# Kernel optimization log

Hardware: AMD Instinct MI355X
Metric: run time of the kernel (lower is better)

## Reference

```python
import jax, jax.numpy as jnp
import numpy as np

B, T, D = 64, 256, 1024   # batch, seq_len, input_dim (== hidden_dim)
H = 1024                  # hidden_dim
L = 4                     # layer_dim
O = 512                   # output_dim


def setup_inputs() -> dict:
    key = jax.random.key(0)
    ks = jax.random.split(key, 8)
    s = 1.0 / np.sqrt(H)  # torch LSTMCell default init scale
    u = lambda k, shape: jax.random.uniform(k, shape, jnp.float32, -s, s)
    return {
        "x": jax.random.normal(ks[0], (B, T, D), jnp.float32),
        "W_ih": u(ks[1], (L, 4 * H, D)),   # layer 0 input dim == H
        "W_hh": u(ks[2], (L, 4 * H, H)),
        "b_ih": u(ks[3], (L, 4 * H)),
        "b_hh": u(ks[4], (L, 4 * H)),
        "W_fc": u(ks[5], (O, H)),
        "b_fc": u(ks[6], (O,)),
    }


def _lstm_forward(x, W_ih, W_hh, b_ih, b_hh, W_fc, b_fc):
    def step(carry, x_t):
        h, c = carry  # each [L, B, H]
        inp = x_t     # [B, D]
        for l in range(L):
            gates = inp @ W_ih[l].T + b_ih[l] + h[l] @ W_hh[l].T + b_hh[l]  # [B, 4H]
            i, f, g, o = jnp.split(gates, 4, axis=-1)
            i, f, o = jax.nn.sigmoid(i), jax.nn.sigmoid(f), jax.nn.sigmoid(o)
            g = jnp.tanh(g)
            c_new = f * c[l] + i * g
            h_new = o * jnp.tanh(c_new)
            h = h.at[l].set(h_new)
            c = c.at[l].set(c_new)
            inp = h_new
        return (h, c), None

    h0 = jnp.zeros((L, x.shape[0], H), x.dtype)
    c0 = jnp.zeros((L, x.shape[0], H), x.dtype)
    (h, _), _ = jax.lax.scan(step, (h0, c0), jnp.swapaxes(x, 0, 1))  # scan over time
    return h[-1] @ W_fc.T + b_fc  # [B, O]


def reference(x, W_ih, W_hh, b_ih, b_hh, W_fc, b_fc):
    return _lstm_forward(x, W_ih, W_hh, b_ih, b_hh, W_fc, b_fc)
```

## Files before the change

kernel.cpp:

```cpp
#include <hip/hip_runtime.h>


typedef short           bf16x8 __attribute__((ext_vector_type(8)));
typedef unsigned short  u16x8  __attribute__((ext_vector_type(8)));
typedef float           f32x4  __attribute__((ext_vector_type(4)));

static constexpr int kB  = 64;
static constexpr int kT  = 256;
static constexpr int kH  = 1024;
static constexpr int kL  = 4;
static constexpr int kNG = 4096;
static constexpr int kK2 = 2048;

static constexpr size_t OFF_W    = 0;
static constexpr size_t OFF_BIAS = 67108864;
static constexpr size_t OFF_XB   = 67174400;
static constexpr size_t OFF_H    = 100728832;
static constexpr size_t OFF_C    = 101777408;

static __device__ __forceinline__ unsigned short f2bf(float f) {
  unsigned int u = __float_as_uint(f);
  u += 0x7fffu + ((u >> 16) & 1u);
  return (unsigned short)(u >> 16);
}
static __device__ __forceinline__ float bf2f(unsigned short s) {
  return __uint_as_float(((unsigned int)s) << 16);
}
static __device__ __forceinline__ float sigm_(float x) {
  return 1.0f / (1.0f + __expf(-x));
}
static __device__ __forceinline__ float tanh_(float x) {
  return 1.0f - 2.0f / (__expf(2.0f * x) + 1.0f);
}

__global__ __launch_bounds__(256) void prepack_w(const float* __restrict__ Wih,
                                                 const float* __restrict__ Whh,
                                                 unsigned short* __restrict__ Wcat) {
  const size_t total = (size_t)kL * kNG * kK2;
  for (size_t e = (size_t)blockIdx.x * 256 + threadIdx.x; e < total;
       e += (size_t)gridDim.x * 256) {
    int k = (int)(e & 2047);
    int n = (int)((e >> 11) & 4095);
    int l = (int)(e >> 23);
    int r = (n & 3) * 1024 + (n >> 2);
    float v = (k < 1024) ? Wih[((size_t)l * kNG + r) * 1024 + k]
                         : Whh[((size_t)l * kNG + r) * 1024 + (k - 1024)];
    Wcat[e] = f2bf(v);
  }
}

__global__ __launch_bounds__(256) void prepack_bias(const float* __restrict__ bih,
                                                    const float* __restrict__ bhh,
                                                    float* __restrict__ bias) {
  int e = blockIdx.x * 256 + threadIdx.x;
  int l = e >> 12, n = e & 4095;
  int r = (n & 3) * 1024 + (n >> 2);
  bias[e] = bih[l * kNG + r] + bhh[l * kNG + r];
}

__global__ __launch_bounds__(256) void prepack_x(const float* __restrict__ x,
                                                 unsigned short* __restrict__ xb) {
  size_t e = ((size_t)blockIdx.x * 256 + threadIdx.x) * 8;
  float4 f0 = *(const float4*)(x + e);
  float4 f1 = *(const float4*)(x + e + 4);
  u16x8 v;
  v[0] = f2bf(f0.x); v[1] = f2bf(f0.y); v[2] = f2bf(f0.z); v[3] = f2bf(f0.w);
  v[4] = f2bf(f1.x); v[5] = f2bf(f1.y); v[6] = f2bf(f1.z); v[7] = f2bf(f1.w);
  *(u16x8*)(xb + e) = v;
}

__global__ __launch_bounds__(256) void lstm_diag(
    const unsigned short* __restrict__ Wcat, const float* __restrict__ bias,
    const unsigned short* __restrict__ xb, unsigned short* __restrict__ hbuf,
    float* __restrict__ cbuf, int d) {
  const int l = blockIdx.x >> 6;
  const int t = d - l;
  if (t < 0 || t >= kT) return;
  const int nwg = (blockIdx.x & 63) * 64;

  const int tid  = threadIdx.x;
  const int lane = tid & 63;
  const int w    = tid >> 6;
  const int quad = lane >> 4;
  const int l15  = lane & 15;

  const unsigned short* srcA;
  size_t strideA;
  if (w < 2) {
    if (l == 0) { srcA = xb + (size_t)t * kH + w * 512; strideA = (size_t)kT * kH; }
    else {
      srcA = hbuf + (size_t)((t & 1) * kL + (l - 1)) * (kB * kH) + w * 512;
      strideA = kH;
    }
  } else {
    srcA = hbuf + (size_t)(((t + 1) & 1) * kL + l) * (kB * kH) + (w - 2) * 512;
    strideA = kH;
  }

  const unsigned short* pA[4];
  const unsigned short* pB[4];
  {
    const unsigned short* wrow =
        Wcat + ((size_t)(l * kNG + nwg + l15)) * kK2 + w * 512 + quad * 8;
#pragma unroll
    for (int i = 0; i < 4; ++i) {
      pA[i] = srcA + (size_t)(i * 16 + l15) * strideA + quad * 8;
      pB[i] = wrow + (size_t)i * 16 * kK2;
    }
  }

  f32x4 acc[4][4] = {};
  bf16x8 a0[4], b0[4], a1[4], b1[4];

#pragma unroll
  for (int i = 0; i < 4; ++i) { a0[i] = *(const bf16x8*)(pA[i]); b0[i] = *(const bf16x8*)(pB[i]); }

#pragma unroll
  for (int kc = 0; kc < 16; ++kc) {
    bf16x8* ac = (kc & 1) ? a1 : a0;
    bf16x8* bc = (kc & 1) ? b1 : b0;
    bf16x8* an = (kc & 1) ? a0 : a1;
    bf16x8* bn = (kc & 1) ? b0 : b1;
    if (kc < 15) {
#pragma unroll
      for (int i = 0; i < 4; ++i) {
        an[i] = *(const bf16x8*)(pA[i] + (kc + 1) * 32);
        bn[i] = *(const bf16x8*)(pB[i] + (kc + 1) * 32);
      }
    }
#pragma unroll
    for (int mt = 0; mt < 4; ++mt)
#pragma unroll
      for (int nt = 0; nt < 4; ++nt)
        acc[mt][nt] = __builtin_amdgcn_mfma_f32_16x16x32_bf16(ac[mt], bc[nt],
                                                              acc[mt][nt], 0, 0, 0);
  }

  __shared__ float part[2][64][68];

  if (w >= 2) {
    float* p = &part[w - 2][0][0];
#pragma unroll
    for (int mt = 0; mt < 4; ++mt)
#pragma unroll
      for (int nt = 0; nt < 4; ++nt)
#pragma unroll
        for (int r = 0; r < 4; ++r)
          p[(mt * 16 + quad * 4 + r) * 68 + nt * 16 + l15] = acc[mt][nt][r];
  }
  __syncthreads();
  if (w < 2) {
    const float* p = &part[w][0][0];
#pragma unroll
    for (int mt = 0; mt < 4; ++mt)
#pragma unroll
      for (int nt = 0; nt < 4; ++nt)
#pragma unroll
        for (int r = 0; r < 4; ++r)
          acc[mt][nt][r] += p[(mt * 16 + quad * 4 + r) * 68 + nt * 16 + l15];
  }
  __syncthreads();
  if (w < 2) {
    float* p = &part[w][0][0];
#pragma unroll
    for (int mt = 0; mt < 4; ++mt)
#pragma unroll
      for (int nt = 0; nt < 4; ++nt)
#pragma unroll
        for (int r = 0; r < 4; ++r)
          p[(mt * 16 + quad * 4 + r) * 68 + nt * 16 + l15] = acc[mt][nt][r];
  }
  __syncthreads();

  const int m  = (w << 4) | (lane >> 2);
  const int ug = lane & 3;
  unsigned short* hout = hbuf + (size_t)((t & 1) * kL + l) * (kB * kH);
#pragma unroll
  for (int j = 0; j < 4; ++j) {
    int ul = 4 * j + ug;
    int nb = 4 * ul;
    float4 p0 = *(const float4*)&part[0][m][nb];
    float4 p1 = *(const float4*)&part[1][m][nb];
    float4 bs = *(const float4*)&bias[l * kNG + nwg + nb];
    float gi = sigm_(p0.x + p1.x + bs.x);
    float gf = sigm_(p0.y + p1.y + bs.y);
    float gg = tanh_(p0.z + p1.z + bs.z);
    float go = sigm_(p0.w + p1.w + bs.w);
    int u = (nwg >> 2) + ul;
    size_t ci = ((size_t)l * kB + m) * kH + u;
    float cn = gf * cbuf[ci] + gi * gg;
    cbuf[ci] = cn;
    hout[(size_t)m * kH + u] = f2bf(go * tanh_(cn));
  }
}

__global__ __launch_bounds__(256) void lstm_fc(const unsigned short* __restrict__ h3,
                                               const float* __restrict__ Wfc,
                                               const float* __restrict__ bfc,
                                               float* __restrict__ out) {
  int gt = blockIdx.x * 256 + threadIdx.x;
  int b = gt >> 9, o = gt & 511;
  const unsigned short* hr = h3 + (size_t)b * kH;
  const float* wr = Wfc + (size_t)o * kH;
  float acc = bfc[o];
#pragma unroll 4
  for (int k = 0; k < kH; k += 8) {
    u16x8 hv = *(const u16x8*)(hr + k);
    float4 w0 = *(const float4*)(wr + k);
    float4 w1 = *(const float4*)(wr + k + 4);
    acc += bf2f(hv[0]) * w0.x + bf2f(hv[1]) * w0.y + bf2f(hv[2]) * w0.z +
           bf2f(hv[3]) * w0.w + bf2f(hv[4]) * w1.x + bf2f(hv[5]) * w1.y +
           bf2f(hv[6]) * w1.z + bf2f(hv[7]) * w1.w;
  }
  out[gt] = acc;
}

extern "C" void kernel_launch(void* const* d_in, const int* in_sizes, int n_in,
                              void* d_out, int out_size, void* d_ws, size_t ws_size,
                              hipStream_t stream) {
  (void)in_sizes; (void)n_in; (void)out_size; (void)ws_size;
  const float* x   = (const float*)d_in[0];
  const float* Wih = (const float*)d_in[1];
  const float* Whh = (const float*)d_in[2];
  const float* bih = (const float*)d_in[3];
  const float* bhh = (const float*)d_in[4];
  const float* Wfc = (const float*)d_in[5];
  const float* bfc = (const float*)d_in[6];
  float* out = (float*)d_out;

  char* ws = (char*)d_ws;
  unsigned short* Wcat = (unsigned short*)(ws + OFF_W);
  float*          bias = (float*)(ws + OFF_BIAS);
  unsigned short* xb   = (unsigned short*)(ws + OFF_XB);
  unsigned short* hbuf = (unsigned short*)(ws + OFF_H);
  float*          cbuf = (float*)(ws + OFF_C);

  prepack_w<<<8192, 256, 0, stream>>>(Wih, Whh, Wcat);
  prepack_bias<<<64, 256, 0, stream>>>(bih, bhh, bias);
  prepack_x<<<8192, 256, 0, stream>>>(x, xb);
  hipMemsetAsync(ws + OFF_H, 0, 2097152, stream);

  for (int d = 0; d < kT + kL - 1; ++d)
    lstm_diag<<<256, 256, 0, stream>>>(Wcat, bias, xb, hbuf, cbuf, d);

  lstm_fc<<<128, 256, 0, stream>>>(hbuf + (size_t)7 * kB * kH, Wfc, bfc, out);
}
```

Before: 5.969 ms.

## Replace per-diagonal launches with persistent register-resident-weight LSTM kernel using flag sync

```diff
diff --git a/kernel.cpp b/kernel.cpp
--- a/kernel.cpp
+++ b/kernel.cpp
@@ -10,52 +10,21 @@
 static constexpr int kH  = 1024;
 static constexpr int kL  = 4;
 static constexpr int kNG = 4096;
-static constexpr int kK2 = 2048;
-
-static constexpr size_t OFF_W    = 0;
-static constexpr size_t OFF_BIAS = 67108864;
-static constexpr size_t OFF_XB   = 67174400;
-static constexpr size_t OFF_H    = 100728832;
-static constexpr size_t OFF_C    = 101777408;
+
+static constexpr size_t OFF_XB   = 0;
+static constexpr size_t OFF_H    = 33554432;
+static constexpr size_t OFF_FLAG = 35651584;
 
 static __device__ __forceinline__ unsigned short f2bf(float f) {
   unsigned int u = __float_as_uint(f);
   u += 0x7fffu + ((u >> 16) & 1u);
   return (unsigned short)(u >> 16);
 }
-static __device__ __forceinline__ float bf2f(unsigned short s) {
-  return __uint_as_float(((unsigned int)s) << 16);
-}
 static __device__ __forceinline__ float sigm_(float x) {
   return 1.0f / (1.0f + __expf(-x));
 }
 static __device__ __forceinline__ float tanh_(float x) {
   return 1.0f - 2.0f / (__expf(2.0f * x) + 1.0f);
-}
-
-__global__ __launch_bounds__(256) void prepack_w(const float* __restrict__ Wih,
-                                                 const float* __restrict__ Whh,
-                                                 unsigned short* __restrict__ Wcat) {
-  const size_t total = (size_t)kL * kNG * kK2;
-  for (size_t e = (size_t)blockIdx.x * 256 + threadIdx.x; e < total;
-       e += (size_t)gridDim.x * 256) {
-    int k = (int)(e & 2047);
-    int n = (int)((e >> 11) & 4095);
-    int l = (int)(e >> 23);
-    int r = (n & 3) * 1024 + (n >> 2);
-    float v = (k < 1024) ? Wih[((size_t)l * kNG + r) * 1024 + k]
-                         : Whh[((size_t)l * kNG + r) * 1024 + (k - 1024)];
-    Wcat[e] = f2bf(v);
-  }
-}
-
-__global__ __launch_bounds__(256) void prepack_bias(const float* __restrict__ bih,
-                                                    const float* __restrict__ bhh,
-                                                    float* __restrict__ bias) {
-  int e = blockIdx.x * 256 + threadIdx.x;
-  int l = e >> 12, n = e & 4095;
-  int r = (n & 3) * 1024 + (n >> 2);
-  bias[e] = bih[l * kNG + r] + bhh[l * kNG + r];
 }
 
 __global__ __launch_bounds__(256) void prepack_x(const float* __restrict__ x,
@@ -69,128 +38,174 @@
   *(u16x8*)(xb + e) = v;
 }
 
-__global__ __launch_bounds__(256) void lstm_diag(
-    const unsigned short* __restrict__ Wcat, const float* __restrict__ bias,
+__global__ __launch_bounds__(256, 1) void lstm_persist(
+    const float* __restrict__ Wih, const float* __restrict__ Whh,
+    const float* __restrict__ bih, const float* __restrict__ bhh,
     const unsigned short* __restrict__ xb, unsigned short* __restrict__ hbuf,
-    float* __restrict__ cbuf, int d) {
-  const int l = blockIdx.x >> 6;
-  const int t = d - l;
-  if (t < 0 || t >= kT) return;
-  const int nwg = (blockIdx.x & 63) * 64;
-
+    int* __restrict__ flags) {
+  const int l    = blockIdx.x >> 6;
+  const int nwg  = (blockIdx.x & 63) * 64;
   const int tid  = threadIdx.x;
   const int lane = tid & 63;
   const int w    = tid >> 6;
   const int quad = lane >> 4;
   const int l15  = lane & 15;
 
-  const unsigned short* srcA;
-  size_t strideA;
-  if (w < 2) {
-    if (l == 0) { srcA = xb + (size_t)t * kH + w * 512; strideA = (size_t)kT * kH; }
-    else {
-      srcA = hbuf + (size_t)((t & 1) * kL + (l - 1)) * (kB * kH) + w * 512;
-      strideA = kH;
-    }
-  } else {
-    srcA = hbuf + (size_t)(((t + 1) & 1) * kL + l) * (kB * kH) + (w - 2) * 512;
-    strideA = kH;
-  }
-
-  const unsigned short* pA[4];
-  const unsigned short* pB[4];
+  __shared__ float part[2][64][68];
+  __shared__ float cst[16][66];
+
+  for (int i = tid; i < 16 * 66; i += 256) (&cst[0][0])[i] = 0.0f;
+
+  bf16x8 wreg[16][4];
   {
-    const unsigned short* wrow =
-        Wcat + ((size_t)(l * kNG + nwg + l15)) * kK2 + w * 512 + quad * 8;
-#pragma unroll
-    for (int i = 0; i < 4; ++i) {
-      pA[i] = srcA + (size_t)(i * 16 + l15) * strideA + quad * 8;
-      pB[i] = wrow + (size_t)i * 16 * kK2;
-    }
-  }
-
-  f32x4 acc[4][4] = {};
-  bf16x8 a0[4], b0[4], a1[4], b1[4];
-
-#pragma unroll
-  for (int i = 0; i < 4; ++i) { a0[i] = *(const bf16x8*)(pA[i]); b0[i] = *(const bf16x8*)(pB[i]); }
-
-#pragma unroll
-  for (int kc = 0; kc < 16; ++kc) {
-    bf16x8* ac = (kc & 1) ? a1 : a0;
-    bf16x8* bc = (kc & 1) ? b1 : b0;
-    bf16x8* an = (kc & 1) ? a0 : a1;
-    bf16x8* bn = (kc & 1) ? b0 : b1;
-    if (kc < 15) {
-#pragma unroll
-      for (int i = 0; i < 4; ++i) {
-        an[i] = *(const bf16x8*)(pA[i] + (kc + 1) * 32);
-        bn[i] = *(const bf16x8*)(pB[i] + (kc + 1) * 32);
+    const float* Wsrc = (w < 2) ? Wih : Whh;
+    const int kofs = (w < 2) ? w * 512 : (w - 2) * 512;
+#pragma unroll
+    for (int nt = 0; nt < 4; ++nt) {
+      int n = nwg + nt * 16 + l15;
+      int r = (n & 3) * 1024 + (n >> 2);
+      const float* src = Wsrc + ((size_t)l * kNG + r) * 1024 + kofs + quad * 8;
+#pragma unroll
+      for (int kc = 0; kc < 16; ++kc) {
+        float4 f0 = *(const float4*)(src + kc * 32);
+        float4 f1 = *(const float4*)(src + kc * 32 + 4);
+        bf16x8 v;
+        v[0] = (short)f2bf(f0.x); v[1] = (short)f2bf(f0.y);
+        v[2] = (short)f2bf(f0.z); v[3] = (short)f2bf(f0.w);
+        v[4] = (short)f2bf(f1.x); v[5] = (short)f2bf(f1.y);
+        v[6] = (short)f2bf(f1.z); v[7] = (short)f2bf(f1.w);
+        wreg[kc][nt] = v;
       }
     }
-#pragma unroll
-    for (int mt = 0; mt < 4; ++mt)
-#pragma unroll
-      for (int nt = 0; nt < 4; ++nt)
-        acc[mt][nt] = __builtin_amdgcn_mfma_f32_16x16x32_bf16(ac[mt], bc[nt],
-                                                              acc[mt][nt], 0, 0, 0);
-  }
-
-  __shared__ float part[2][64][68];
-
-  if (w >= 2) {
-    float* p = &part[w - 2][0][0];
-#pragma unroll
-    for (int mt = 0; mt < 4; ++mt)
-#pragma unroll
-      for (int nt = 0; nt < 4; ++nt)
-#pragma unroll
-        for (int r = 0; r < 4; ++r)
-          p[(mt * 16 + quad * 4 + r) * 68 + nt * 16 + l15] = acc[mt][nt][r];
-  }
-  __syncthreads();
-  if (w < 2) {
-    const float* p = &part[w][0][0];
-#pragma unroll
-    for (int mt = 0; mt < 4; ++mt)
-#pragma unroll
-      for (int nt = 0; nt < 4; ++nt)
-#pragma unroll
-        for (int r = 0; r < 4; ++r)
-          acc[mt][nt][r] += p[(mt * 16 + quad * 4 + r) * 68 + nt * 16 + l15];
-  }
-  __syncthreads();
-  if (w < 2) {
-    float* p = &part[w][0][0];
-#pragma unroll
-    for (int mt = 0; mt < 4; ++mt)
-#pragma unroll
-      for (int nt = 0; nt < 4; ++nt)
-#pragma unroll
-        for (int r = 0; r < 4; ++r)
-          p[(mt * 16 + quad * 4 + r) * 68 + nt * 16 + l15] = acc[mt][nt][r];
-  }
-  __syncthreads();
-
-  const int m  = (w << 4) | (lane >> 2);
-  const int ug = lane & 3;
-  unsigned short* hout = hbuf + (size_t)((t & 1) * kL + l) * (kB * kH);
+  }
+
+  const int m_ep = (w << 4) | (lane >> 2);
+  const int ug   = lane & 3;
+  float4 bs4[4];
 #pragma unroll
   for (int j = 0; j < 4; ++j) {
-    int ul = 4 * j + ug;
-    int nb = 4 * ul;
-    float4 p0 = *(const float4*)&part[0][m][nb];
-    float4 p1 = *(const float4*)&part[1][m][nb];
-    float4 bs = *(const float4*)&bias[l * kNG + nwg + nb];
-    float gi = sigm_(p0.x + p1.x + bs.x);
-    float gf = sigm_(p0.y + p1.y + bs.y);
-    float gg = tanh_(p0.z + p1.z + bs.z);
-    float go = sigm_(p0.w + p1.w + bs.w);
-    int u = (nwg >> 2) + ul;
-    size_t ci = ((size_t)l * kB + m) * kH + u;
-    float cn = gf * cbuf[ci] + gi * gg;
-    cbuf[ci] = cn;
-    hout[(size_t)m * kH + u] = f2bf(go * tanh_(cn));
+    int u = (nwg >> 2) + 4 * j + ug;
+    bs4[j].x = bih[l * kNG + u]        + bhh[l * kNG + u];
+    bs4[j].y = bih[l * kNG + 1024 + u] + bhh[l * kNG + 1024 + u];
+    bs4[j].z = bih[l * kNG + 2048 + u] + bhh[l * kNG + 2048 + u];
+    bs4[j].w = bih[l * kNG + 3072 + u] + bhh[l * kNG + 3072 + u];
+  }
+
+  for (int t = 0; t < kT; ++t) {
+    if (l > 0) {
+      const int idx = (l - 1) * kT + t;
+      while (__hip_atomic_load(&flags[idx], __ATOMIC_RELAXED,
+                               __HIP_MEMORY_SCOPE_AGENT) < 64)
+        __builtin_amdgcn_s_sleep(1);
+      (void)__hip_atomic_load(&flags[idx], __ATOMIC_ACQUIRE,
+                              __HIP_MEMORY_SCOPE_AGENT);
+    }
+    if (t > 0) {
+      const int idx = l * kT + t - 1;
+      while (__hip_atomic_load(&flags[idx], __ATOMIC_RELAXED,
+                               __HIP_MEMORY_SCOPE_AGENT) < 64)
+        __builtin_amdgcn_s_sleep(1);
+      (void)__hip_atomic_load(&flags[idx], __ATOMIC_ACQUIRE,
+                              __HIP_MEMORY_SCOPE_AGENT);
+    }
+    if (l < 3 && t >= 4) {
+      const int idx = (l + 1) * kT + t - 4;
+      while (__hip_atomic_load(&flags[idx], __ATOMIC_RELAXED,
+                               __HIP_MEMORY_SCOPE_AGENT) < 64)
+        __builtin_amdgcn_s_sleep(1);
+      (void)__hip_atomic_load(&flags[idx], __ATOMIC_ACQUIRE,
+                              __HIP_MEMORY_SCOPE_AGENT);
+    }
+
+    f32x4 acc[4][4] = {};
+    const bool active = (w < 2) || (t > 0);
+    if (active) {
+      const unsigned short* srcA;
+      size_t strideA;
+      if (w < 2) {
+        if (l == 0) {
+          srcA = xb + (size_t)t * kH + w * 512;
+          strideA = (size_t)kT * kH;
+        } else {
+          srcA = hbuf + (size_t)((t & 3) * kL + (l - 1)) * (kB * kH) + w * 512;
+          strideA = kH;
+        }
+      } else {
+        srcA = hbuf + (size_t)(((t - 1) & 3) * kL + l) * (kB * kH) + (w - 2) * 512;
+        strideA = kH;
+      }
+      const unsigned short* pA[4];
+#pragma unroll
+      for (int i = 0; i < 4; ++i)
+        pA[i] = srcA + (size_t)(i * 16 + l15) * strideA + quad * 8;
+
+      bf16x8 abuf[4][4];
+#pragma unroll
+      for (int p = 0; p < 3; ++p)
+#pragma unroll
+        for (int i = 0; i < 4; ++i)
+          abuf[p][i] = *(const bf16x8*)(pA[i] + p * 32);
+#pragma unroll
+      for (int kc = 0; kc < 16; ++kc) {
+        if (kc < 13) {
+#pragma unroll
+          for (int i = 0; i < 4; ++i)
+            abuf[(kc + 3) & 3][i] = *(const bf16x8*)(pA[i] + (kc + 3) * 32);
+        }
+#pragma unroll
+        for (int mt = 0; mt < 4; ++mt)
+#pragma unroll
+          for (int nt = 0; nt < 4; ++nt)
+            acc[mt][nt] = __builtin_amdgcn_mfma_f32_16x16x32_bf16(
+                abuf[kc & 3][mt], wreg[kc][nt], acc[mt][nt], 0, 0, 0);
+      }
+    }
+
+    if (w >= 2) {
+      float* p = &part[w - 2][0][0];
+#pragma unroll
+      for (int mt = 0; mt < 4; ++mt)
+#pragma unroll
+        for (int nt = 0; nt < 4; ++nt)
+#pragma unroll
+          for (int r = 0; r < 4; ++r)
+            p[(mt * 16 + quad * 4 + r) * 68 + nt * 16 + l15] = acc[mt][nt][r];
+    }
+    __syncthreads();
+    if (w < 2) {
+      float* p = &part[w][0][0];
+#pragma unroll
+      for (int mt = 0; mt < 4; ++mt)
+#pragma unroll
+        for (int nt = 0; nt < 4; ++nt)
+#pragma unroll
+          for (int r = 0; r < 4; ++r) {
+            int a = (mt * 16 + quad * 4 + r) * 68 + nt * 16 + l15;
+            p[a] += acc[mt][nt][r];
+          }
+    }
+    __syncthreads();
+
+    unsigned short* hout = hbuf + (size_t)((t & 3) * kL + l) * (kB * kH);
+#pragma unroll
+    for (int j = 0; j < 4; ++j) {
+      int ul = 4 * j + ug;
+      int nb = 4 * ul;
+      float4 p0 = *(const float4*)&part[0][m_ep][nb];
+      float4 p1 = *(const float4*)&part[1][m_ep][nb];
+      float gi = sigm_(p0.x + p1.x + bs4[j].x);
+      float gf = sigm_(p0.y + p1.y + bs4[j].y);
+      float gg = tanh_(p0.z + p1.z + bs4[j].z);
+      float go = sigm_(p0.w + p1.w + bs4[j].w);
+      float cn = gf * cst[ul][m_ep] + gi * gg;
+      cst[ul][m_ep] = cn;
+      hout[(size_t)m_ep * kH + (nwg >> 2) + ul] = f2bf(go * tanh_(cn));
+    }
+
+    __syncthreads();
+    if (tid == 0)
+      __hip_atomic_fetch_add(&flags[l * kT + t], 1, __ATOMIC_RELEASE,
+                             __HIP_MEMORY_SCOPE_AGENT);
   }
 }
 
@@ -208,9 +223,14 @@
     u16x8 hv = *(const u16x8*)(hr + k);
     float4 w0 = *(const float4*)(wr + k);
     float4 w1 = *(const float4*)(wr + k + 4);
-    acc += bf2f(hv[0]) * w0.x + bf2f(hv[1]) * w0.y + bf2f(hv[2]) * w0.z +
-           bf2f(hv[3]) * w0.w + bf2f(hv[4]) * w1.x + bf2f(hv[5]) * w1.y +
-           bf2f(hv[6]) * w1.z + bf2f(hv[7]) * w1.w;
+    acc += __uint_as_float((unsigned)hv[0] << 16) * w0.x +
+           __uint_as_float((unsigned)hv[1] << 16) * w0.y +
+           __uint_as_float((unsigned)hv[2] << 16) * w0.z +
+           __uint_as_float((unsigned)hv[3] << 16) * w0.w +
+           __uint_as_float((unsigned)hv[4] << 16) * w1.x +
+           __uint_as_float((unsigned)hv[5] << 16) * w1.y +
+           __uint_as_float((unsigned)hv[6] << 16) * w1.z +
+           __uint_as_float((unsigned)hv[7] << 16) * w1.w;
   }
   out[gt] = acc;
 }
@@ -229,19 +249,15 @@
   float* out = (float*)d_out;
 
   char* ws = (char*)d_ws;
-  unsigned short* Wcat = (unsigned short*)(ws + OFF_W);
-  float*          bias = (float*)(ws + OFF_BIAS);
-  unsigned short* xb   = (unsigned short*)(ws + OFF_XB);
-  unsigned short* hbuf = (unsigned short*)(ws + OFF_H);
-  float*          cbuf = (float*)(ws + OFF_C);
-
-  prepack_w<<<8192, 256, 0, stream>>>(Wih, Whh, Wcat);
-  prepack_bias<<<64, 256, 0, stream>>>(bih, bhh, bias);
+  unsigned short* xb    = (unsigned short*)(ws + OFF_XB);
+  unsigned short* hbuf  = (unsigned short*)(ws + OFF_H);
+  int*            flags = (int*)(ws + OFF_FLAG);
+
   prepack_x<<<8192, 256, 0, stream>>>(x, xb);
-  hipMemsetAsync(ws + OFF_H, 0, 2097152, stream);
-
-  for (int d = 0; d < kT + kL - 1; ++d)
-    lstm_diag<<<256, 256, 0, stream>>>(Wcat, bias, xb, hbuf, cbuf, d);
-
-  lstm_fc<<<128, 256, 0, stream>>>(hbuf + (size_t)7 * kB * kH, Wfc, bfc, out);
-}
+  hipMemsetAsync(ws + OFF_FLAG, 0, kL * kT * sizeof(int), stream);
+
+  lstm_persist<<<256, 256, 0, stream>>>(Wih, Whh, bih, bhh, xb, hbuf, flags);
+
+  lstm_fc<<<128, 256, 0, stream>>>(hbuf + (size_t)(3 * kL + 3) * kB * kH,
+                                   Wfc, bfc, out);
+}
```

Result: slower. 11.28 ms (+88.9%).
